# Kernel tuning notes

Measured on AMD Instinct MI355X. Metric: run time of the kernel, lower is better.

## Reference

```python
import jax, jax.numpy as jnp
import numpy as np

B, S, E, H = 2, 2048, 1024, 16
DK = E // H  # 64


def setup_inputs() -> dict:
    key = jax.random.key(0)
    ks = jax.random.split(key, 5)
    scale = 1.0 / np.sqrt(E)
    return {
        "x": jax.random.normal(ks[0], (B, S, E), dtype=jnp.float32),
        "Wq": jax.random.normal(ks[1], (E, E), dtype=jnp.float32) * scale,
        "Wk": jax.random.normal(ks[2], (E, E), dtype=jnp.float32) * scale,
        "Wv": jax.random.normal(ks[3], (E, E), dtype=jnp.float32) * scale,
        "Wo": jax.random.normal(ks[4], (E, E), dtype=jnp.float32) * scale,
    }


def reference(x, Wq, Wk, Wv, Wo):
    # Linear layers: y = x @ W.T (torch nn.Linear convention, bias=False)
    b, s, e = x.shape
    q = (x @ Wq.T).reshape(b, s, H, DK)  # (B,S,H,dk)
    k = (x @ Wk.T).reshape(b, s, H, DK)
    v = (x @ Wv.T).reshape(b, s, H, DK)
    # scores = Q K^T / sqrt(d_k)  -> (B,H,Sq,Sk)
    scores = jnp.einsum("bihd,bkhd->bhik", q, k) / jnp.sqrt(jnp.asarray(DK, x.dtype))
    p = jax.nn.softmax(scores, axis=-1)
    # dropout is identity in eval/deterministic mode
    attn = jnp.einsum("bhik,bkhd->bihd", p, v)  # (B,S,H,dk)
    concat = attn.reshape(b, s, e)
    return concat @ Wo.T
```

## Files before the change

kernel.cpp:

```cpp
#include <hip/hip_runtime.h>
#include <hip/hip_bf16.h>
#include <cstdint>
#include <cstddef>

typedef __bf16 bf16_t;
typedef __attribute__((ext_vector_type(8))) __bf16 bf16x8;
typedef __attribute__((ext_vector_type(4))) __bf16 bf16x4;
typedef __attribute__((ext_vector_type(4))) float f32x4;
typedef __attribute__((ext_vector_type(16))) float f32x16;
typedef uint32_t u32;
typedef __attribute__((ext_vector_type(4))) u32 u32x4;
typedef __attribute__((ext_vector_type(2))) u32 u32x2;

constexpr int B_ = 2, S_ = 2048, E_ = 1024, H_ = 16, DK_ = 64;

__device__ __forceinline__ void gl2lds16(const void* g, void* l) {
  __builtin_amdgcn_global_load_lds(
      (const __attribute__((address_space(1))) void*)g,
      (__attribute__((address_space(3))) void*)l, 16, 0, 0);
}

__device__ __forceinline__ float exp2_(float x) {
#if __has_builtin(__builtin_amdgcn_exp2f)
  return __builtin_amdgcn_exp2f(x);
#else
  return exp2f(x);
#endif
}

__device__ __forceinline__ u32 cvtpk(float lo, float hi) {
  u32 r;
  asm("v_cvt_pk_bf16_f32 %0, %1, %2" : "=v"(r) : "v"(lo), "v"(hi));
  return r;
}

__device__ __forceinline__ void pl32swap(u32& a, u32& b) {
#if __has_builtin(__builtin_amdgcn_permlane32_swap)
  const u32x2 r = __builtin_amdgcn_permlane32_swap(a, b, false, false);
  a = r[0]; b = r[1];
#else
  asm volatile("v_permlane32_swap_b32 %0, %1" : "+v"(a), "+v"(b));
#endif
}

__device__ __forceinline__ float xmax32(float v) {
  u32 a = __builtin_bit_cast(u32, v), b = a;
  pl32swap(a, b);
  return fmaxf(__builtin_bit_cast(float, a), __builtin_bit_cast(float, b));
}
__device__ __forceinline__ float xadd32(float v) {
  u32 a = __builtin_bit_cast(u32, v), b = a;
  pl32swap(a, b);
  return __builtin_bit_cast(float, a) + __builtin_bit_cast(float, b);
}

__device__ __forceinline__ bf16x8 ldsfrag(const char* base, int row, int chunk) {
  return *reinterpret_cast<const bf16x8*>(base + row * 128 + (((chunk ^ (row & 7))) << 4));
}

__global__ __launch_bounds__(256) void f2bf_kernel(const float* __restrict__ in,
                                                   bf16_t* __restrict__ out, int n4) {
  int i = blockIdx.x * 256 + threadIdx.x;
  if (i >= n4) return;
  const float4 v = reinterpret_cast<const float4*>(in)[i];
  bf16x4 o;
  o[0] = (bf16_t)v.x; o[1] = (bf16_t)v.y; o[2] = (bf16_t)v.z; o[3] = (bf16_t)v.w;
  reinterpret_cast<bf16x4*>(out)[i] = o;
}

__global__ __launch_bounds__(256) void f2bf_w(const float* __restrict__ w0,
                                              const float* __restrict__ w1,
                                              const float* __restrict__ w2,
                                              const float* __restrict__ w3,
                                              bf16_t* __restrict__ out) {
  const int i = blockIdx.x * 256 + threadIdx.x;
  const int seg = i >> 18, off = i & 262143;
  const float* src = seg == 0 ? w0 : seg == 1 ? w1 : seg == 2 ? w2 : w3;
  const float4 v = reinterpret_cast<const float4*>(src)[off];
  bf16x4 o;
  o[0] = (bf16_t)v.x; o[1] = (bf16_t)v.y; o[2] = (bf16_t)v.z; o[3] = (bf16_t)v.w;
  reinterpret_cast<bf16x4*>(out)[i] = o;
}

__global__ __launch_bounds__(256) void gemm_qkv(const bf16_t* __restrict__ A,
                                                const bf16_t* __restrict__ Bt,
                                                bf16_t* __restrict__ Qo,
                                                bf16_t* __restrict__ Ko,
                                                bf16_t* __restrict__ Vto,
                                                int K, float qscale) {
  __shared__ bf16_t As[128 * 32];
  __shared__ bf16_t Bs[128 * 32];
  const int tid = threadIdx.x;
  const int w = tid >> 6, l = tid & 63;
  const int wr = w >> 1, wc = w & 1;
  const int tm = blockIdx.x * 128, tn = blockIdx.y * 128;
  f32x4 acc[4][4] = {};

  for (int k0 = 0; k0 < K; k0 += 32) {
#pragma unroll
    for (int i = 0; i < 2; ++i) {
      const int r = i * 64 + w * 16 + (l >> 2);
      const int c = k0 + (l & 3) * 8;
      gl2lds16(A + (size_t)(tm + r) * K + c, As + (i * 64 + w * 16) * 32);
      gl2lds16(Bt + (size_t)(tn + r) * K + c, Bs + (i * 64 + w * 16) * 32);
    }
    __syncthreads();

    bf16x8 af[4], bfr[4];
#pragma unroll
    for (int mi = 0; mi < 4; ++mi)
      af[mi] = *reinterpret_cast<const bf16x8*>(
          As + (wr * 64 + mi * 16 + (l & 15)) * 32 + (l >> 4) * 8);
#pragma unroll
    for (int ni = 0; ni < 4; ++ni)
      bfr[ni] = *reinterpret_cast<const bf16x8*>(
          Bs + (wc * 64 + ni * 16 + (l & 15)) * 32 + (l >> 4) * 8);
#pragma unroll
    for (int mi = 0; mi < 4; ++mi)
#pragma unroll
      for (int ni = 0; ni < 4; ++ni)
        acc[mi][ni] =
            __builtin_amdgcn_mfma_f32_16x16x32_bf16(af[mi], bfr[ni], acc[mi][ni], 0, 0, 0);
    __syncthreads();
  }

#pragma unroll
  for (int mi = 0; mi < 4; ++mi)
#pragma unroll
    for (int ni = 0; ni < 4; ++ni) {
      if (tn < 2048) {
        bf16_t* C = (tn < 1024) ? Qo : Ko;
        const float sc = (tn < 1024) ? qscale : 1.0f;
        const int colb = (tn < 1024) ? tn : tn - 1024;
#pragma unroll
        for (int r = 0; r < 4; ++r) {
          const int row = tm + wr * 64 + mi * 16 + (l >> 4) * 4 + r;
          const int col = colb + wc * 64 + ni * 16 + (l & 15);
          C[(size_t)row * 1024 + col] = (bf16_t)(acc[mi][ni][r] * sc);
        }
      } else {
        const int tok0 = tm + wr * 64 + mi * 16 + (l >> 4) * 4;
        const int feat = (tn - 2048) + wc * 64 + ni * 16 + (l & 15);
        const int b = tok0 >> 11, s = tok0 & 2047;
        bf16x4 o4;
#pragma unroll
        for (int r = 0; r < 4; ++r) o4[r] = (bf16_t)acc[mi][ni][r];
        *reinterpret_cast<bf16x4*>(Vto + (((size_t)(b * E_ + feat)) << 11) + s) = o4;
      }
    }
}

__global__ __launch_bounds__(256) void gemm_o(const bf16_t* __restrict__ A,
                                              const bf16_t* __restrict__ Bt,
                                              float* __restrict__ C,
                                              int M, int N, int K) {
  __shared__ bf16_t As[64 * 32];
  __shared__ bf16_t Bs[128 * 32];
  const int tid = threadIdx.x;
  const int w = tid >> 6, l = tid & 63;
  const int wr = w >> 1, wc = w & 1;
  const int tm = blockIdx.x * 64, tn = blockIdx.y * 128;
  f32x4 acc[2][4] = {};

  for (int k0 = 0; k0 < K; k0 += 32) {
    const int c = k0 + (l & 3) * 8;
    gl2lds16(A + (size_t)(tm + w * 16 + (l >> 2)) * K + c, As + (w * 16) * 32);
#pragma unroll
    for (int i = 0; i < 2; ++i)
      gl2lds16(Bt + (size_t)(tn + i * 64 + w * 16 + (l >> 2)) * K + c,
               Bs + (i * 64 + w * 16) * 32);
    __syncthreads();

    bf16x8 af[2], bfr[4];
#pragma unroll
    for (int mi = 0; mi < 2; ++mi)
      af[mi] = *reinterpret_cast<const bf16x8*>(
          As + (wr * 32 + mi * 16 + (l & 15)) * 32 + (l >> 4) * 8);
#pragma unroll
    for (int ni = 0; ni < 4; ++ni)
      bfr[ni] = *reinterpret_cast<const bf16x8*>(
          Bs + (wc * 64 + ni * 16 + (l & 15)) * 32 + (l >> 4) * 8);
#pragma unroll
    for (int mi = 0; mi < 2; ++mi)
#pragma unroll
      for (int ni = 0; ni < 4; ++ni)
        acc[mi][ni] =
            __builtin_amdgcn_mfma_f32_16x16x32_bf16(af[mi], bfr[ni], acc[mi][ni], 0, 0, 0);
    __syncthreads();
  }

#pragma unroll
  for (int mi = 0; mi < 2; ++mi)
#pragma unroll
    for (int ni = 0; ni < 4; ++ni)
#pragma unroll
      for (int r = 0; r < 4; ++r) {
        const int row = tm + wr * 32 + mi * 16 + (l >> 4) * 4 + r;
        const int col = tn + wc * 64 + ni * 16 + (l & 15);
        C[(size_t)row * N + col] = acc[mi][ni][r];
      }
}

template <int SPLIT>
__global__ __launch_bounds__(128, 2) void attn_fwd(const bf16_t* __restrict__ Q,
                                                   const bf16_t* __restrict__ K,
                                                   const bf16_t* __restrict__ Vt,
                                                   bf16_t* __restrict__ O,
                                                   float* __restrict__ Op,
                                                   float2* __restrict__ mlbuf) {
  __shared__ __align__(16) char smem[33280];
  const int tid = threadIdx.x;
  const int w = tid >> 6, l = tid & 63;
  const int hi = l >> 5;
  const int nblk = SPLIT ? 1024 : 512;
  const int flat = blockIdx.x + (blockIdx.y << 4) + (blockIdx.z << 9);
  const int wid = (flat & 7) * (nblk >> 3) + (flat >> 3);
  const int qb = wid & 15, bh = (wid >> 4) & 31;
  const int half = SPLIT ? (wid >> 9) : 0;
  const int q0 = qb * 128 + w * 64;
  const size_t hb = (size_t)(bh >> 4) * (S_ * E_) + (size_t)(bh & 15) * DK_;
  const bf16_t* const Qh = Q + hb;
  const bf16_t* const Kh = K + hb;
  const bf16_t* const Vth = Vt + (size_t)bh * (DK_ * S_);

  float* const Lb = (float*)(smem + 32768) + w * 64;

  const int srow = l >> 3;
  const int schunk = (l & 7) ^ srow;

  bf16x8 qf[2][4];
#pragma unroll
  for (int qn = 0; qn < 2; ++qn)
#pragma unroll
    for (int df = 0; df < 4; ++df)
      qf[qn][df] = *reinterpret_cast<const bf16x8*>(
          Qh + (size_t)(q0 + qn * 32 + (l & 31)) * E_ + df * 16 + hi * 8);

  f32x16 oacc[2][2] = {};
  float m0 = -INFINITY, m1 = -INFINITY, l0 = 0.f, l1 = 0.f;

  auto stage = [&](int t, int buf) {
    const int t0 = t * 64;
#pragma unroll
    for (int c = 0; c < 4; ++c) {
      const int rg = c * 2 + w;
      const int row = rg * 8 + srow;
      gl2lds16(Kh + (size_t)(t0 + row) * E_ + schunk * 8,
               smem + buf * 8192 + rg * 1024);
      gl2lds16(Vth + (size_t)row * S_ + t0 + schunk * 8,
               smem + 16384 + buf * 8192 + rg * 1024);
    }
  };

  const int tbeg = SPLIT ? half * 16 : 0;
  const int ntl = SPLIT ? 16 : 32;

  stage(tbeg, 0);
  __syncthreads();

  for (int tt = 0; tt < ntl; ++tt) {
    const int cur = tt & 1;
    if (tt < ntl - 1) stage(tbeg + tt + 1, cur ^ 1);
    const char* const Kcur = smem + cur * 8192;
    const char* const Vcur = smem + 16384 + cur * 8192;

    f32x16 sacc[2][2] = {};
    __builtin_amdgcn_s_setprio(1);
#pragma unroll
    for (int kb = 0; kb < 2; ++kb)
#pragma unroll
      for (int df = 0; df < 4; ++df) {
        const bf16x8 kf = ldsfrag(Kcur, kb * 32 + (l & 31), df * 2 + hi);
        sacc[0][kb] = __builtin_amdgcn_mfma_f32_32x32x16_bf16(kf, qf[0][df], sacc[0][kb], 0, 0, 0);
        sacc[1][kb] = __builtin_amdgcn_mfma_f32_32x32x16_bf16(kf, qf[1][df], sacc[1][kb], 0, 0, 0);
      }
    __builtin_amdgcn_s_setprio(0);

    float pmax0, pmax1;
    {
      float t8a[8], t8b[8];
#pragma unroll
      for (int u = 0; u < 8; ++u) {
        t8a[u] = fmaxf(fmaxf(sacc[0][0][u], sacc[0][0][u + 8]),
                       fmaxf(sacc[0][1][u], sacc[0][1][u + 8]));
        t8b[u] = fmaxf(fmaxf(sacc[1][0][u], sacc[1][0][u + 8]),
                       fmaxf(sacc[1][1][u], sacc[1][1][u + 8]));
      }
#pragma unroll
      for (int u = 0; u < 4; ++u) {
        t8a[u] = fmaxf(t8a[u], t8a[u + 4]);
        t8b[u] = fmaxf(t8b[u], t8b[u + 4]);
      }
      pmax0 = xmax32(fmaxf(fmaxf(t8a[0], t8a[1]), fmaxf(t8a[2], t8a[3])));
      pmax1 = xmax32(fmaxf(fmaxf(t8b[0], t8b[1]), fmaxf(t8b[2], t8b[3])));
    }
    const bool ok = (pmax0 <= m0 + 8.f) && (pmax1 <= m1 + 8.f);
    if (!__all(ok)) {
      const float mn0 = fmaxf(m0, pmax0), mn1 = fmaxf(m1, pmax1);
      const float a0 = exp2_(m0 - mn0), a1 = exp2_(m1 - mn1);
      m0 = mn0; m1 = mn1; l0 *= a0; l1 *= a1;
      if (l < 32) { Lb[l] = a0; Lb[32 + l] = a1; }
#pragma unroll
      for (int qn = 0; qn < 2; ++qn)
#pragma unroll
        for (int g = 0; g < 4; ++g) {
          const f32x4 av = *reinterpret_cast<const f32x4*>(Lb + qn * 32 + g * 8 + hi * 4);
#pragma unroll
          for (int dn = 0; dn < 2; ++dn)
#pragma unroll
            for (int j = 0; j < 4; ++j) oacc[qn][dn][g * 4 + j] *= av[j];
        }
    }
#pragma unroll
    for (int kb = 0; kb < 2; ++kb)
#pragma unroll
      for (int u = 0; u < 16; ++u) {
        sacc[0][kb][u] = exp2_(sacc[0][kb][u] - m0);
        sacc[1][kb][u] = exp2_(sacc[1][kb][u] - m1);
      }
    {
      float a8[8], b8[8];
#pragma unroll
      for (int u = 0; u < 8; ++u) {
        a8[u] = (sacc[0][0][u] + sacc[0][0][u + 8]) + (sacc[0][1][u] + sacc[0][1][u + 8]);
        b8[u] = (sacc[1][0][u] + sacc[1][0][u + 8]) + (sacc[1][1][u] + sacc[1][1][u + 8]);
      }
#pragma unroll
      for (int u = 0; u < 4; ++u) { a8[u] += a8[u + 4]; b8[u] += b8[u + 4]; }
      l0 += xadd32((a8[0] + a8[1]) + (a8[2] + a8[3]));
      l1 += xadd32((b8[0] + b8[1]) + (b8[2] + b8[3]));
    }

#pragma unroll
    for (int kf = 0; kf < 4; ++kf) {
      const int kb = kf >> 1, u0 = (kf & 1) * 8;
      bf16x8 pa[2];
#pragma unroll
      for (int qn = 0; qn < 2; ++qn) {
        u32 w0 = cvtpk(sacc[qn][kb][u0 + 0], sacc[qn][kb][u0 + 1]);
        u32 w1 = cvtpk(sacc[qn][kb][u0 + 2], sacc[qn][kb][u0 + 3]);
        u32 w2 = cvtpk(sacc[qn][kb][u0 + 4], sacc[qn][kb][u0 + 5]);
        u32 w3 = cvtpk(sacc[qn][kb][u0 + 6], sacc[qn][kb][u0 + 7]);
        pl32swap(w0, w2);
        pl32swap(w1, w3);
        u32x4 pw; pw[0] = w0; pw[1] = w1; pw[2] = w2; pw[3] = w3;
        pa[qn] = __builtin_bit_cast(bf16x8, pw);
      }
      __builtin_amdgcn_s_setprio(1);
#pragma unroll
      for (int dn = 0; dn < 2; ++dn) {
        const bf16x8 vf = ldsfrag(Vcur, dn * 32 + (l & 31), kf * 2 + hi);
        oacc[0][dn] = __builtin_amdgcn_mfma_f32_32x32x16_bf16(pa[0], vf, oacc[0][dn], 0, 0, 0);
        oacc[1][dn] = __builtin_amdgcn_mfma_f32_32x32x16_bf16(pa[1], vf, oacc[1][dn], 0, 0, 0);
      }
      __builtin_amdgcn_s_setprio(0);
    }
    __syncthreads();
  }

  if constexpr (SPLIT) {
    const int rbase = bh * S_ + q0;
    float* const Oph = Op + ((size_t)half << 22);
    if (l < 32) {
      mlbuf[(half << 16) + rbase + l] = make_float2(m0, l0);
      mlbuf[(half << 16) + rbase + 32 + l] = make_float2(m1, l1);
    }
#pragma unroll
    for (int qn = 0; qn < 2; ++qn)
#pragma unroll
      for (int g = 0; g < 4; ++g)
#pragma unroll
        for (int j = 0; j < 4; ++j) {
          const int q = q0 + qn * 32 + g * 8 + hi * 4 + j;
          float* const dst = Oph + (size_t)(bh * S_ + q) * 64 + (l & 31);
          dst[0]  = oacc[qn][0][g * 4 + j];
          dst[32] = oacc[qn][1][g * 4 + j];
        }
  } else {
    if (l < 32) { Lb[l] = 1.f / l0; Lb[32 + l] = 1.f / l1; }
#pragma unroll
    for (int qn = 0; qn < 2; ++qn)
#pragma unroll
      for (int g = 0; g < 4; ++g) {
        const f32x4 iv = *reinterpret_cast<const f32x4*>(Lb + qn * 32 + g * 8 + hi * 4);
#pragma unroll
        for (int dn = 0; dn < 2; ++dn)
#pragma unroll
          for (int j = 0; j < 4; ++j) {
            const int q = q0 + qn * 32 + g * 8 + hi * 4 + j;
            O[hb + (size_t)q * E_ + dn * 32 + (l & 31)] =
                (bf16_t)(oacc[qn][dn][g * 4 + j] * iv[j]);
          }
      }
  }
}

__global__ __launch_bounds__(256) void attn_combine(const float* __restrict__ Op,
                                                    const float2* __restrict__ ml,
                                                    bf16_t* __restrict__ Ac) {
  const int idx = blockIdx.x * 256 + threadIdx.x;
  const int r = idx >> 4, c4 = idx & 15;
  const float2 e0 = ml[r], e1 = ml[65536 + r];
  const float m = fmaxf(e0.x, e1.x);
  const float a0 = exp2f(e0.x - m), a1 = exp2f(e1.x - m);
  const float inv = 1.f / (e0.y * a0 + e1.y * a1);
  const f32x4 o0 = reinterpret_cast<const f32x4*>(Op)[(size_t)r * 16 + c4];
  const f32x4 o1 = reinterpret_cast<const f32x4*>(Op + (1u << 22))[(size_t)r * 16 + c4];
  const int q = r & 2047, bh = r >> 11;
  bf16x4 o;
#pragma unroll
  for (int j = 0; j < 4; ++j) o[j] = (bf16_t)((o0[j] * a0 + o1[j] * a1) * inv);
  *reinterpret_cast<bf16x4*>(Ac + (size_t)(bh >> 4) * (S_ * E_) + (size_t)q * E_ +
                             (bh & 15) * DK_ + c4 * 4) = o;
}

extern "C" void kernel_launch(void* const* d_in, const int* in_sizes, int n_in,
                              void* d_out, int out_size, void* d_ws, size_t ws_size,
                              hipStream_t stream) {
  const float* x  = (const float*)d_in[0];
  const float* Wq = (const float*)d_in[1];
  const float* Wk = (const float*)d_in[2];
  const float* Wv = (const float*)d_in[3];
  const float* Wo = (const float*)d_in[4];
  float* out = (float*)d_out;

  bf16_t* xb  = (bf16_t*)d_ws;
  bf16_t* wqb = xb + 4194304;
  bf16_t* wob = wqb + 3145728;
  bf16_t* Qb  = wqb + 4194304;
  bf16_t* Kb  = Qb + 4194304;
  bf16_t* Vtb = Kb + 4194304;
  float*  Opart = (float*)(Vtb + 4194304);
  float2* mlbuf = (float2*)(Opart + 8388608);
  bf16_t* Ac = xb;

  const bool split = ws_size >= 76546048ull;

  f2bf_kernel<<<4096, 256, 0, stream>>>(x, xb, 1048576);
  f2bf_w<<<4096, 256, 0, stream>>>(Wq, Wk, Wv, Wo, wqb);

  gemm_qkv<<<dim3(32, 24), 256, 0, stream>>>(xb, wqb, Qb, Kb, Vtb, 1024, 0.18033688f);

  if (split) {
    attn_fwd<1><<<dim3(16, 32, 2), 128, 0, stream>>>(Qb, Kb, Vtb, nullptr, Opart, mlbuf);
    attn_combine<<<4096, 256, 0, stream>>>(Opart, mlbuf, Ac);
  } else {
    attn_fwd<0><<<dim3(16, 32, 1), 128, 0, stream>>>(Qb, Kb, Vtb, Ac, nullptr, nullptr);
  }

  gemm_o<<<dim3(64, 8), 256, 0, stream>>>(Ac, wob, out, 4096, 1024, 1024);
}
```

Measured before the change: 133.2 us.

## Load K/V tiles directly into registers instead of LDS double-buffering in attention

The attention kernel stops staging K and V tiles through shared memory with global_load_lds and barriers. Each wave now loads its own K and V MFMA fragments straight from global memory into registers and prefetches the next tile after using the current one. Blocks grow to four independent waves, and the partial-output layout and combine kernel change to float2 interleaved stores. This removes LDS traffic and __syncthreads, but every wave now fetches K/V separately, which raises global/L2 traffic and register pressure.

```diff
diff --git a/kernel.cpp b/kernel.cpp
--- a/kernel.cpp
+++ b/kernel.cpp
@@ -52,10 +52,6 @@
   u32 a = __builtin_bit_cast(u32, v), b = a;
   pl32swap(a, b);
   return __builtin_bit_cast(float, a) + __builtin_bit_cast(float, b);
-}
-
-__device__ __forceinline__ bf16x8 ldsfrag(const char* base, int row, int chunk) {
-  return *reinterpret_cast<const bf16x8*>(base + row * 128 + (((chunk ^ (row & 7))) << 4));
 }
 
 __global__ __launch_bounds__(256) void f2bf_kernel(const float* __restrict__ in,
@@ -202,31 +198,31 @@
 }
 
 template <int SPLIT>
-__global__ __launch_bounds__(128, 2) void attn_fwd(const bf16_t* __restrict__ Q,
+__global__ __launch_bounds__(256, 2) void attn_fwd(const bf16_t* __restrict__ Q,
                                                    const bf16_t* __restrict__ K,
                                                    const bf16_t* __restrict__ Vt,
                                                    bf16_t* __restrict__ O,
                                                    float* __restrict__ Op,
                                                    float2* __restrict__ mlbuf) {
-  __shared__ __align__(16) char smem[33280];
+  __shared__ float LbAll[4 * 64];
   const int tid = threadIdx.x;
   const int w = tid >> 6, l = tid & 63;
-  const int hi = l >> 5;
-  const int nblk = SPLIT ? 1024 : 512;
-  const int flat = blockIdx.x + (blockIdx.y << 4) + (blockIdx.z << 9);
+  const int hi = l >> 5, l31 = l & 31;
+  const int nblk = SPLIT ? 512 : 256;
+  const int flat = blockIdx.x;
   const int wid = (flat & 7) * (nblk >> 3) + (flat >> 3);
-  const int qb = wid & 15, bh = (wid >> 4) & 31;
-  const int half = SPLIT ? (wid >> 9) : 0;
-  const int q0 = qb * 128 + w * 64;
+  const int gw = wid * 4 + w;
+  const int qb = gw & 31, bh = (gw >> 5) & 31;
+  const int half = SPLIT ? (gw >> 10) : 0;
+  const int q0 = qb * 64;
   const size_t hb = (size_t)(bh >> 4) * (S_ * E_) + (size_t)(bh & 15) * DK_;
   const bf16_t* const Qh = Q + hb;
   const bf16_t* const Kh = K + hb;
   const bf16_t* const Vth = Vt + (size_t)bh * (DK_ * S_);
-
-  float* const Lb = (float*)(smem + 32768) + w * 64;
-
-  const int srow = l >> 3;
-  const int schunk = (l & 7) ^ srow;
+  float* const Lb = LbAll + w * 64;
+
+  const bf16_t* const Kbase = Kh + (size_t)l31 * E_ + hi * 8;
+  const bf16_t* const Vbase = Vth + (size_t)l31 * S_ + hi * 8;
 
   bf16x8 qf[2][4];
 #pragma unroll
@@ -234,35 +230,30 @@
 #pragma unroll
     for (int df = 0; df < 4; ++df)
       qf[qn][df] = *reinterpret_cast<const bf16x8*>(
-          Qh + (size_t)(q0 + qn * 32 + (l & 31)) * E_ + df * 16 + hi * 8);
+          Qh + (size_t)(q0 + qn * 32 + l31) * E_ + df * 16 + hi * 8);
 
   f32x16 oacc[2][2] = {};
   float m0 = -INFINITY, m1 = -INFINITY, l0 = 0.f, l1 = 0.f;
 
-  auto stage = [&](int t, int buf) {
-    const int t0 = t * 64;
-#pragma unroll
-    for (int c = 0; c < 4; ++c) {
-      const int rg = c * 2 + w;
-      const int row = rg * 8 + srow;
-      gl2lds16(Kh + (size_t)(t0 + row) * E_ + schunk * 8,
-               smem + buf * 8192 + rg * 1024);
-      gl2lds16(Vth + (size_t)row * S_ + t0 + schunk * 8,
-               smem + 16384 + buf * 8192 + rg * 1024);
-    }
-  };
-
   const int tbeg = SPLIT ? half * 16 : 0;
   const int ntl = SPLIT ? 16 : 32;
 
-  stage(tbeg, 0);
-  __syncthreads();
+  bf16x8 kreg[2][4], vreg[2][4];
+#pragma unroll
+  for (int kb = 0; kb < 2; ++kb)
+#pragma unroll
+    for (int df = 0; df < 4; ++df)
+      kreg[kb][df] = *reinterpret_cast<const bf16x8*>(
+          Kbase + (size_t)(tbeg * 64 + kb * 32) * E_ + df * 16);
+#pragma unroll
+  for (int dn = 0; dn < 2; ++dn)
+#pragma unroll
+    for (int kf = 0; kf < 4; ++kf)
+      vreg[dn][kf] = *reinterpret_cast<const bf16x8*>(
+          Vbase + (size_t)dn * 32 * S_ + tbeg * 64 + kf * 16);
 
   for (int tt = 0; tt < ntl; ++tt) {
-    const int cur = tt & 1;
-    if (tt < ntl - 1) stage(tbeg + tt + 1, cur ^ 1);
-    const char* const Kcur = smem + cur * 8192;
-    const char* const Vcur = smem + 16384 + cur * 8192;
+    const int tn64 = (tt < ntl - 1 ? tbeg + tt + 1 : tbeg + tt) * 64;
 
     f32x16 sacc[2][2] = {};
     __builtin_amdgcn_s_setprio(1);
@@ -270,11 +261,17 @@
     for (int kb = 0; kb < 2; ++kb)
 #pragma unroll
       for (int df = 0; df < 4; ++df) {
-        const bf16x8 kf = ldsfrag(Kcur, kb * 32 + (l & 31), df * 2 + hi);
-        sacc[0][kb] = __builtin_amdgcn_mfma_f32_32x32x16_bf16(kf, qf[0][df], sacc[0][kb], 0, 0, 0);
-        sacc[1][kb] = __builtin_amdgcn_mfma_f32_32x32x16_bf16(kf, qf[1][df], sacc[1][kb], 0, 0, 0);
+        sacc[0][kb] = __builtin_amdgcn_mfma_f32_32x32x16_bf16(kreg[kb][df], qf[0][df], sacc[0][kb], 0, 0, 0);
+        sacc[1][kb] = __builtin_amdgcn_mfma_f32_32x32x16_bf16(kreg[kb][df], qf[1][df], sacc[1][kb], 0, 0, 0);
       }
     __builtin_amdgcn_s_setprio(0);
+
+#pragma unroll
+    for (int kb = 0; kb < 2; ++kb)
+#pragma unroll
+      for (int df = 0; df < 4; ++df)
+        kreg[kb][df] = *reinterpret_cast<const bf16x8*>(
+            Kbase + (size_t)(tn64 + kb * 32) * E_ + df * 16);
 
     float pmax0, pmax1;
     {
@@ -349,33 +346,34 @@
       __builtin_amdgcn_s_setprio(1);
 #pragma unroll
       for (int dn = 0; dn < 2; ++dn) {
-        const bf16x8 vf = ldsfrag(Vcur, dn * 32 + (l & 31), kf * 2 + hi);
-        oacc[0][dn] = __builtin_amdgcn_mfma_f32_32x32x16_bf16(pa[0], vf, oacc[0][dn], 0, 0, 0);
-        oacc[1][dn] = __builtin_amdgcn_mfma_f32_32x32x16_bf16(pa[1], vf, oacc[1][dn], 0, 0, 0);
+        oacc[0][dn] = __builtin_amdgcn_mfma_f32_32x32x16_bf16(pa[0], vreg[dn][kf], oacc[0][dn], 0, 0, 0);
+        oacc[1][dn] = __builtin_amdgcn_mfma_f32_32x32x16_bf16(pa[1], vreg[dn][kf], oacc[1][dn], 0, 0, 0);
       }
       __builtin_amdgcn_s_setprio(0);
     }
-    __syncthreads();
+
+#pragma unroll
+    for (int dn = 0; dn < 2; ++dn)
+#pragma unroll
+      for (int kf = 0; kf < 4; ++kf)
+        vreg[dn][kf] = *reinterpret_cast<const bf16x8*>(
+            Vbase + (size_t)dn * 32 * S_ + tn64 + kf * 16);
   }
 
   if constexpr (SPLIT) {
-    const int rbase = bh * S_ + q0;
     float* const Oph = Op + ((size_t)half << 22);
     if (l < 32) {
-      mlbuf[(half << 16) + rbase + l] = make_float2(m0, l0);
-      mlbuf[(half << 16) + rbase + 32 + l] = make_float2(m1, l1);
+      mlbuf[(half << 16) + bh * S_ + q0 + l] = make_float2(m0, l0);
+      mlbuf[(half << 16) + bh * S_ + q0 + 32 + l] = make_float2(m1, l1);
     }
 #pragma unroll
     for (int qn = 0; qn < 2; ++qn)
 #pragma unroll
-      for (int g = 0; g < 4; ++g)
-#pragma unroll
-        for (int j = 0; j < 4; ++j) {
-          const int q = q0 + qn * 32 + g * 8 + hi * 4 + j;
-          float* const dst = Oph + (size_t)(bh * S_ + q) * 64 + (l & 31);
-          dst[0]  = oacc[qn][0][g * 4 + j];
-          dst[32] = oacc[qn][1][g * 4 + j];
-        }
+      for (int u = 0; u < 16; ++u) {
+        const int q = q0 + qn * 32 + (u & 3) + 8 * (u >> 2) + 4 * hi;
+        *reinterpret_cast<float2*>(Oph + (size_t)(bh * S_ + q) * 64 + l31 * 2) =
+            make_float2(oacc[qn][0][u], oacc[qn][1][u]);
+      }
   } else {
     if (l < 32) { Lb[l] = 1.f / l0; Lb[32 + l] = 1.f / l1; }
 #pragma unroll
@@ -388,7 +386,7 @@
 #pragma unroll
           for (int j = 0; j < 4; ++j) {
             const int q = q0 + qn * 32 + g * 8 + hi * 4 + j;
-            O[hb + (size_t)q * E_ + dn * 32 + (l & 31)] =
+            O[hb + (size_t)q * E_ + dn * 32 + l31] =
                 (bf16_t)(oacc[qn][dn][g * 4 + j] * iv[j]);
           }
       }
@@ -399,19 +397,18 @@
                                                     const float2* __restrict__ ml,
                                                     bf16_t* __restrict__ Ac) {
   const int idx = blockIdx.x * 256 + threadIdx.x;
-  const int r = idx >> 4, c4 = idx & 15;
+  const int r = idx >> 5, c = idx & 31;
   const float2 e0 = ml[r], e1 = ml[65536 + r];
   const float m = fmaxf(e0.x, e1.x);
   const float a0 = exp2f(e0.x - m), a1 = exp2f(e1.x - m);
   const float inv = 1.f / (e0.y * a0 + e1.y * a1);
-  const f32x4 o0 = reinterpret_cast<const f32x4*>(Op)[(size_t)r * 16 + c4];
-  const f32x4 o1 = reinterpret_cast<const f32x4*>(Op + (1u << 22))[(size_t)r * 16 + c4];
+  const float2 p0 = *reinterpret_cast<const float2*>(Op + (size_t)r * 64 + c * 2);
+  const float2 p1 = *reinterpret_cast<const float2*>(Op + (1u << 22) + (size_t)r * 64 + c * 2);
   const int q = r & 2047, bh = r >> 11;
-  bf16x4 o;
-#pragma unroll
-  for (int j = 0; j < 4; ++j) o[j] = (bf16_t)((o0[j] * a0 + o1[j] * a1) * inv);
-  *reinterpret_cast<bf16x4*>(Ac + (size_t)(bh >> 4) * (S_ * E_) + (size_t)q * E_ +
-                             (bh & 15) * DK_ + c4 * 4) = o;
+  bf16_t* const base =
+      Ac + (size_t)(bh >> 4) * (S_ * E_) + (size_t)q * E_ + (bh & 15) * DK_;
+  base[c] = (bf16_t)((p0.x * a0 + p1.x * a1) * inv);
+  base[c + 32] = (bf16_t)((p0.y * a0 + p1.y * a1) * inv);
 }
 
 extern "C" void kernel_launch(void* const* d_in, const int* in_sizes, int n_in,
@@ -442,10 +439,10 @@
   gemm_qkv<<<dim3(32, 24), 256, 0, stream>>>(xb, wqb, Qb, Kb, Vtb, 1024, 0.18033688f);
 
   if (split) {
-    attn_fwd<1><<<dim3(16, 32, 2), 128, 0, stream>>>(Qb, Kb, Vtb, nullptr, Opart, mlbuf);
-    attn_combine<<<4096, 256, 0, stream>>>(Opart, mlbuf, Ac);
+    attn_fwd<1><<<512, 256, 0, stream>>>(Qb, Kb, Vtb, nullptr, Opart, mlbuf);
+    attn_combine<<<8192, 256, 0, stream>>>(Opart, mlbuf, Ac);
   } else {
-    attn_fwd<0><<<dim3(16, 32, 1), 128, 0, stream>>>(Qb, Kb, Vtb, Ac, nullptr, nullptr);
+    attn_fwd<0><<<256, 256, 0, stream>>>(Qb, Kb, Vtb, Ac, nullptr, nullptr);
   }
 
   gemm_o<<<dim3(64, 8), 256, 0, stream>>>(Ac, wob, out, 4096, 1024, 1024);
```

After: 153.8 us. 15.5% more time.
